# Optimization experiments

Hardware: AMD Instinct MI355X
Metric: run time of the kernel (lower is better)

## Reference

```python
import jax, jax.numpy as jnp
import numpy as np

N, D_IN, F = 65536, 512, 256
E = 524288
BATCH, K1 = 32, 200
BN_EPS = 1e-5


def setup_inputs() -> dict:
    key = jax.random.key(0)
    ks = iter(jax.random.split(key, 64))

    def nrm(shape, s=0.05):
        return jax.random.normal(next(ks), shape, jnp.float32) * s

    inp = {
        "feat": jax.random.normal(next(ks), (N, D_IN), jnp.float32),
        "A": jax.random.randint(next(ks), (2, E), 0, N, dtype=jnp.int32),
        "h1id": jax.random.randint(next(ks), (BATCH * K1,), 0, N // BATCH, dtype=jnp.int32),
        "batch": BATCH,
    }
    dims = [(D_IN, F), (F, F), (F, F), (F, F)]
    for i, (di, do) in enumerate(dims, 1):
        inp[f"eps{i}"] = jnp.zeros((), jnp.float32)          # GINConv train_eps, init 0
        inp[f"w{i}a"] = nrm((di, do)); inp[f"b{i}a"] = jnp.zeros((do,), jnp.float32)
        inp[f"w{i}b"] = nrm((do, do)); inp[f"b{i}b"] = jnp.zeros((do,), jnp.float32)
        inp[f"g{i}"] = jnp.ones((do,), jnp.float32)          # BN gamma
        inp[f"be{i}"] = jnp.zeros((do,), jnp.float32)        # BN beta
        inp[f"m{i}"] = nrm((do,))                            # BN running mean
        inp[f"v{i}"] = jax.random.uniform(next(ks), (do,), jnp.float32, 0.5, 1.5)  # BN running var
    inp["wc1"] = nrm((F, F)); inp["bc1"] = jnp.zeros((F,), jnp.float32)
    inp["pa"] = jnp.full((F,), 0.25, jnp.float32)            # PReLU per-channel slope
    inp["wc2"] = nrm((F, 2)); inp["bc2"] = jnp.zeros((2,), jnp.float32)
    return inp


def _gin_conv(x, src, dst, eps, wa, ba, wb, bb, g, be, m, v):
    # sum aggregation over in-edges: aggr[i] = sum_{(j->i)} x[j]
    aggr = jax.ops.segment_sum(x[src], dst, num_segments=N)
    h = (1.0 + eps) * x + aggr
    h = jax.nn.relu(h @ wa + ba) @ wb + bb
    # BatchNorm1d in eval mode (running stats)
    return (h - m) * jax.lax.rsqrt(v + BN_EPS) * g + be


def _forward(feat, A, h1id, batch,
             eps1, w1a, b1a, w1b, b1b, g1, be1, m1, v1,
             eps2, w2a, b2a, w2b, b2b, g2, be2, m2, v2,
             eps3, w3a, b3a, w3b, b3b, g3, be3, m3, v3,
             eps4, w4a, b4a, w4b, b4b, g4, be4, m4, v4,
             wc1, bc1, pa, wc2, bc2):
    src, dst = A[0], A[1]
    h = jax.nn.relu(_gin_conv(feat, src, dst, eps1, w1a, b1a, w1b, b1b, g1, be1, m1, v1))
    h = jax.nn.relu(_gin_conv(h, src, dst, eps2, w2a, b2a, w2b, b2b, g2, be2, m2, v2))
    h = jax.nn.relu(_gin_conv(h, src, dst, eps3, w3a, b3a, w3b, b3b, g3, be3, m3, v3))
    h = _gin_conv(h, src, dst, eps4, w4a, b4a, w4b, b4b, g4, be4, m4, v4)
    score = h.reshape(batch, -1, F)                      # [B, n_per_graph, F]
    idx = h1id.reshape(batch, K1)
    edge_feat = jnp.take_along_axis(score, idx[:, :, None], axis=1)  # [B, K1, F]
    ef = edge_feat.reshape(-1, F)
    hc = ef @ wc1 + bc1
    hc = jnp.where(hc > 0, hc, pa * hc)                  # PReLU(256)
    return hc @ wc2 + bc2                                # [B*K1, 2]


def reference(feat, A, h1id, batch,
              eps1, w1a, b1a, w1b, b1b, g1, be1, m1, v1,
              eps2, w2a, b2a, w2b, b2b, g2, be2, m2, v2,
              eps3, w3a, b3a, w3b, b3b, g3, be3, m3, v3,
              eps4, w4a, b4a, w4b, b4b, g4, be4, m4, v4,
              wc1, bc1, pa, wc2, bc2):
    return _forward(feat, A, h1id, batch,
                    eps1, w1a, b1a, w1b, b1b, g1, be1, m1, v1,
                    eps2, w2a, b2a, w2b, b2b, g2, be2, m2, v2,
                    eps3, w3a, b3a, w3b, b3b, g3, be3, m3, v3,
                    eps4, w4a, b4a, w4b, b4b, g4, be4, m4, v4,
                    wc1, bc1, pa, wc2, bc2)
```

## Files before the change

### kernel.cpp

```cpp
#include <hip/hip_runtime.h>

typedef unsigned short u16;
typedef unsigned int   u32;
typedef __bf16  bf16x8 __attribute__((ext_vector_type(8)));
typedef float   f32x4  __attribute__((ext_vector_type(4)));
typedef u32     u32x4  __attribute__((ext_vector_type(4)));

#define NN 65536
#define NE 524288
#define FD 256

typedef const __attribute__((address_space(1))) void* gas_p;
typedef __attribute__((address_space(3))) void* las_p;
#define GLDS16(g, l) __builtin_amdgcn_global_load_lds((gas_p)(const void*)(g), (las_p)(void*)(l), 16, 0, 0)

__device__ __forceinline__ u16 f2bf(float f){
  u32 u = __float_as_uint(f);
  u += 0x7fffu + ((u >> 16) & 1u);
  return (u16)(u >> 16);
}
__device__ __forceinline__ float bf2f(u32 lo16){
  return __uint_as_float(lo16 << 16);
}
__device__ __forceinline__ void acc8(float* a, uint4 v){
  a[0] += bf2f(v.x & 0xffffu); a[1] += bf2f(v.x >> 16);
  a[2] += bf2f(v.y & 0xffffu); a[3] += bf2f(v.y >> 16);
  a[4] += bf2f(v.z & 0xffffu); a[5] += bf2f(v.z >> 16);
  a[6] += bf2f(v.w & 0xffffu); a[7] += bf2f(v.w >> 16);
}

__global__ __launch_bounds__(256) void prep_k(
    const float* __restrict__ w1a, const float* __restrict__ w1b,
    const float* __restrict__ w2a, const float* __restrict__ w2b,
    const float* __restrict__ w3a, const float* __restrict__ w3b,
    const float* __restrict__ w4a, const float* __restrict__ w4b,
    const float* __restrict__ wc1, u16* __restrict__ wT)
{
  int idx = blockIdx.x * 256 + threadIdx.x;
  const float* src; int base, K, local;
  if (idx < 131072){ src = w1a; base = 0; K = 512; local = idx; }
  else {
    local = idx - 131072;
    int j = local >> 16;
    local &= 65535;
    K = 256;
    base = 131072 + j * 65536;
    switch (j){
      case 0: src = w1b; break;
      case 1: src = w2a; break;
      case 2: src = w2b; break;
      case 3: src = w3a; break;
      case 4: src = w3b; break;
      case 5: src = w4a; break;
      case 6: src = w4b; break;
      default: src = wc1; break;
    }
  }
  int n = local & 255;
  int k = local >> 8;
  wT[base + n * K + k] = f2bf(src[k * 256 + n]);
}

__global__ __launch_bounds__(256) void hist_k(const int* __restrict__ dst, int* __restrict__ deg){
  int e = blockIdx.x * 256 + threadIdx.x;
  atomicAdd(&deg[dst[e]], 1);
}

__global__ __launch_bounds__(1024) void scan_k(const int* __restrict__ deg, int* __restrict__ rs){
  __shared__ int part[1024];
  int t = threadIdx.x;
  int base = t * 64;
  int sum = 0;
  for (int i = 0; i < 64; ++i) sum += deg[base + i];
  part[t] = sum;
  __syncthreads();
  for (int off = 1; off < 1024; off <<= 1){
    int v = 0;
    if (t >= off) v = part[t - off];
    __syncthreads();
    part[t] += v;
    __syncthreads();
  }
  int run = part[t] - sum;
  for (int i = 0; i < 64; ++i){ rs[base + i] = run; run += deg[base + i]; }
  if (t == 1023) rs[65536] = part[1023];
}

__global__ __launch_bounds__(256) void scat_k(
    const int* __restrict__ src, const int* __restrict__ dst,
    const int* __restrict__ rs, int* __restrict__ cursor, int* __restrict__ csr)
{
  int e = blockIdx.x * 256 + threadIdx.x;
  int d = dst[e];
  int pos = atomicAdd(&cursor[d], 1);
  csr[rs[d] + pos] = src[e];
}

template<int AF32, int MODE, int RELU, int K>
__global__ __launch_bounds__(512) void gemm_k(
    const void* __restrict__ Ap, const u16* __restrict__ Bt,
    u16* __restrict__ C,
    const float* __restrict__ p0, const float* __restrict__ p1,
    const float* __restrict__ p2, const float* __restrict__ p3,
    const float* __restrict__ p4)
{
  __shared__ u16 lds[32768];
  u16* As = lds;
  u16* Bs = lds + 8192;
  const int t    = threadIdx.x;
  const int lane = t & 63;
  const int w    = t >> 6;
  const int wm   = w & 1;
  const int wn   = w >> 1;
  const int m0   = blockIdx.x * 128;
  const int mrow = lane & 15;
  const int quad = lane >> 4;

  f32x4 acc[4][4];
  const f32x4 zero = {0.f, 0.f, 0.f, 0.f};
  #pragma unroll
  for (int i = 0; i < 4; ++i)
    #pragma unroll
    for (int j = 0; j < 4; ++j) acc[i][j] = zero;

  const u16* Ab = (const u16*)Ap;
  const float* Af = (const float*)Ap;

  for (int k0 = 0; k0 < K; k0 += 64){
    if (AF32){
      #pragma unroll
      for (int i = 0; i < 2; ++i){
        int p   = i * 512 + t;
        int row = p >> 3;
        const float* s = Af + (size_t)(m0 + row) * K + k0 + (p & 7) * 8;
        float4 x0 = *(const float4*)s;
        float4 x1 = *(const float4*)(s + 4);
        union { u32x4 q; u16 h[8]; } u;
        u.h[0] = f2bf(x0.x); u.h[1] = f2bf(x0.y); u.h[2] = f2bf(x0.z); u.h[3] = f2bf(x0.w);
        u.h[4] = f2bf(x1.x); u.h[5] = f2bf(x1.y); u.h[6] = f2bf(x1.z); u.h[7] = f2bf(x1.w);
        int dst = (p & ~7) | ((p & 7) ^ (row & 7));
        *(u32x4*)&As[dst * 8] = u.q;
      }
    } else {
      #pragma unroll
      for (int i = 0; i < 2; ++i){
        int p   = i * 512 + t;
        int row = p >> 3;
        int ch  = (p & 7) ^ (row & 7);
        GLDS16(Ab + (size_t)(m0 + row) * K + k0 + ch * 8, &As[p * 8]);
      }
    }
    #pragma unroll
    for (int i = 0; i < 4; ++i){
      int p   = i * 512 + t;
      int row = p >> 3;
      int ch  = (p & 7) ^ (row & 7);
      GLDS16(Bt + (size_t)row * K + k0 + ch * 8, &Bs[p * 8]);
    }
    __syncthreads();
    #pragma unroll
    for (int ks = 0; ks < 2; ++ks){
      bf16x8 af[4], bq[4];
      #pragma unroll
      for (int mi = 0; mi < 4; ++mi){
        int r  = wm * 64 + mi * 16 + mrow;
        int ch = (quad + ks * 4) ^ (r & 7);
        af[mi] = *(const bf16x8*)&As[(r * 8 + ch) * 8];
      }
      #pragma unroll
      for (int ni = 0; ni < 4; ++ni){
        int rb = wn * 64 + ni * 16 + mrow;
        int ch = (quad + ks * 4) ^ (rb & 7);
        bq[ni] = *(const bf16x8*)&Bs[(rb * 8 + ch) * 8];
      }
      #pragma unroll
      for (int mi = 0; mi < 4; ++mi)
        #pragma unroll
        for (int ni = 0; ni < 4; ++ni)
          acc[mi][ni] = __builtin_amdgcn_mfma_f32_16x16x32_bf16(af[mi], bq[ni], acc[mi][ni], 0, 0, 0);
    }
    __syncthreads();
  }

  #pragma unroll
  for (int ni = 0; ni < 4; ++ni){
    int c  = wn * 64 + ni * 16 + mrow;
    float scale = 1.f, shift = 0.f, slope = 0.f;
    if (MODE == 1){
      float s = p0[c] * rsqrtf(p3[c] + 1e-5f);
      scale = s;
      shift = (p4[c] - p2[c]) * s + p1[c];
    }
    if (MODE == 2){ shift = p0[c]; slope = p1[c]; }
    #pragma unroll
    for (int mi = 0; mi < 4; ++mi){
      int rbase = wm * 64 + mi * 16 + quad * 4;
      #pragma unroll
      for (int reg = 0; reg < 4; ++reg){
        float v = acc[mi][ni][reg];
        if (MODE == 1){
          v = v * scale + shift;
          if (RELU) v = fmaxf(v, 0.f);
        }
        if (MODE == 2){
          v += shift;
          v = v > 0.f ? v : slope * v;
        }
        lds[(rbase + reg) * 256 + c] = f2bf(v);
      }
    }
  }
  __syncthreads();
  #pragma unroll
  for (int i = 0; i < 8; ++i){
    int p  = i * 512 + t;
    int r  = p >> 5;
    int ch = p & 31;
    u32x4 q = *(const u32x4*)&lds[r * 256 + ch * 8];
    *(u32x4*)&C[(size_t)(m0 + r) * 256 + ch * 8] = q;
  }
}

__global__ __launch_bounds__(512) void fuse_k(
    const u16* __restrict__ y, const int* __restrict__ rs, const int* __restrict__ csr,
    const float* __restrict__ epsp, const float* __restrict__ abias,
    const u16* __restrict__ B1t,
    const float* __restrict__ g, const float* __restrict__ be,
    const float* __restrict__ m, const float* __restrict__ v,
    const float* __restrict__ bb,
    const u16* __restrict__ B2t,
    u16* __restrict__ yout)
{
  __shared__ u16 lds[32768];
  const int t    = threadIdx.x;
  const int lane = t & 63;
  const int w    = t >> 6;
  const int wm   = w & 1;
  const int wn   = w >> 1;
  const int m0   = blockIdx.x * 128;
  const int mrow = lane & 15;
  const int quad = lane >> 4;

  {
    int lane32 = lane & 31;
    int half   = lane >> 5;
    int f0     = lane32 * 8;
    float e1 = 1.0f + epsp[0];
    float4 b0 = *(const float4*)(abias + f0);
    float4 b1 = *(const float4*)(abias + f0 + 4);
    #pragma unroll 1
    for (int i = 0; i < 8; ++i){
      int r    = w * 16 + i * 2 + half;
      int node = m0 + r;
      int s0 = rs[node], s1 = rs[node + 1];
      float a[8] = {0.f,0.f,0.f,0.f,0.f,0.f,0.f,0.f};
      int e = s0;
      for (; e + 4 <= s1; e += 4){
        int sa = csr[e], sb = csr[e+1], sc = csr[e+2], sd = csr[e+3];
        uint4 va = *(const uint4*)(y + (size_t)sa * 256 + f0);
        uint4 vb = *(const uint4*)(y + (size_t)sb * 256 + f0);
        uint4 vc = *(const uint4*)(y + (size_t)sc * 256 + f0);
        uint4 vd = *(const uint4*)(y + (size_t)sd * 256 + f0);
        acc8(a, va); acc8(a, vb); acc8(a, vc); acc8(a, vd);
      }
      for (; e < s1; ++e)
        acc8(a, *(const uint4*)(y + (size_t)csr[e] * 256 + f0));
      uint4 own = *(const uint4*)(y + (size_t)node * 256 + f0);
      float r0 = fmaxf(e1 * bf2f(own.x & 0xffffu) + a[0] + b0.x, 0.f);
      float r1 = fmaxf(e1 * bf2f(own.x >> 16)     + a[1] + b0.y, 0.f);
      float r2 = fmaxf(e1 * bf2f(own.y & 0xffffu) + a[2] + b0.z, 0.f);
      float r3 = fmaxf(e1 * bf2f(own.y >> 16)     + a[3] + b0.w, 0.f);
      float r4 = fmaxf(e1 * bf2f(own.z & 0xffffu) + a[4] + b1.x, 0.f);
      float r5 = fmaxf(e1 * bf2f(own.z >> 16)     + a[5] + b1.y, 0.f);
      float r6 = fmaxf(e1 * bf2f(own.w & 0xffffu) + a[6] + b1.z, 0.f);
      float r7 = fmaxf(e1 * bf2f(own.w >> 16)     + a[7] + b1.w, 0.f);
      uint4 o;
      o.x = (u32)f2bf(r0) | ((u32)f2bf(r1) << 16);
      o.y = (u32)f2bf(r2) | ((u32)f2bf(r3) << 16);
      o.z = (u32)f2bf(r4) | ((u32)f2bf(r5) << 16);
      o.w = (u32)f2bf(r6) | ((u32)f2bf(r7) << 16);
      int ch = lane32 ^ (r & 7);
      *(uint4*)&lds[r * 256 + ch * 8] = o;
    }
  }
  __syncthreads();

  const f32x4 zero = {0.f, 0.f, 0.f, 0.f};

  f32x4 acc[4][4];
  #pragma unroll
  for (int i = 0; i < 4; ++i)
    #pragma unroll
    for (int j = 0; j < 4; ++j) acc[i][j] = zero;
  #pragma unroll
  for (int ks = 0; ks < 8; ++ks){
    bf16x8 af[4], bq[4];
    #pragma unroll
    for (int mi = 0; mi < 4; ++mi){
      int r    = wm * 64 + mi * 16 + mrow;
      int slot = (ks * 4 + quad) ^ (r & 7);
      af[mi] = *(const bf16x8*)&lds[r * 256 + slot * 8];
    }
    #pragma unroll
    for (int ni = 0; ni < 4; ++ni){
      int rb = wn * 64 + ni * 16 + mrow;
      bq[ni] = *(const bf16x8*)&B1t[(size_t)rb * 256 + ks * 32 + quad * 8];
    }
    #pragma unroll
    for (int mi = 0; mi < 4; ++mi)
      #pragma unroll
      for (int ni = 0; ni < 4; ++ni)
        acc[mi][ni] = __builtin_amdgcn_mfma_f32_16x16x32_bf16(af[mi], bq[ni], acc[mi][ni], 0, 0, 0);
  }
  __syncthreads();

  #pragma unroll
  for (int ni = 0; ni < 4; ++ni){
    int c = wn * 64 + ni * 16 + mrow;
    float scale = g[c] * rsqrtf(v[c] + 1e-5f);
    float shift = (bb[c] - m[c]) * scale + be[c];
    #pragma unroll
    for (int mi = 0; mi < 4; ++mi){
      int rbase = wm * 64 + mi * 16 + quad * 4;
      #pragma unroll
      for (int reg = 0; reg < 4; ++reg){
        int row = rbase + reg;
        float val = fmaxf(acc[mi][ni][reg] * scale + shift, 0.f);
        lds[row * 256 + (((c >> 3) ^ (row & 7)) << 3) + (c & 7)] = f2bf(val);
      }
    }
  }
  __syncthreads();

  f32x4 acc2[4][4];
  #pragma unroll
  for (int i = 0; i < 4; ++i)
    #pragma unroll
    for (int j = 0; j < 4; ++j) acc2[i][j] = zero;
  #pragma unroll
  for (int ks = 0; ks < 8; ++ks){
    bf16x8 af[4], bq[4];
    #pragma unroll
    for (int mi = 0; mi < 4; ++mi){
      int r    = wm * 64 + mi * 16 + mrow;
      int slot = (ks * 4 + quad) ^ (r & 7);
      af[mi] = *(const bf16x8*)&lds[r * 256 + slot * 8];
    }
    #pragma unroll
    for (int ni = 0; ni < 4; ++ni){
      int rb = wn * 64 + ni * 16 + mrow;
      bq[ni] = *(const bf16x8*)&B2t[(size_t)rb * 256 + ks * 32 + quad * 8];
    }
    #pragma unroll
    for (int mi = 0; mi < 4; ++mi)
      #pragma unroll
      for (int ni = 0; ni < 4; ++ni)
        acc2[mi][ni] = __builtin_amdgcn_mfma_f32_16x16x32_bf16(af[mi], bq[ni], acc2[mi][ni], 0, 0, 0);
  }
  __syncthreads();

  #pragma unroll
  for (int ni = 0; ni < 4; ++ni){
    int c = wn * 64 + ni * 16 + mrow;
    #pragma unroll
    for (int mi = 0; mi < 4; ++mi){
      int rbase = wm * 64 + mi * 16 + quad * 4;
      #pragma unroll
      for (int reg = 0; reg < 4; ++reg)
        lds[(rbase + reg) * 256 + c] = f2bf(acc2[mi][ni][reg]);
    }
  }
  __syncthreads();
  #pragma unroll
  for (int i = 0; i < 8; ++i){
    int p  = i * 512 + t;
    int r  = p >> 5;
    int ch = p & 31;
    u32x4 q = *(const u32x4*)&lds[r * 256 + ch * 8];
    *(u32x4*)&yout[(size_t)(m0 + r) * 256 + ch * 8] = q;
  }
}

template<int GATH>
__global__ __launch_bounds__(256) void agg_k(
    const u16* __restrict__ y, const int* __restrict__ rs, const int* __restrict__ csr,
    const float* __restrict__ epsp, const float* __restrict__ bias,
    const int* __restrict__ gidx, u16* __restrict__ tout)
{
  int sub    = threadIdx.x >> 5;
  int lane32 = threadIdx.x & 31;
  int idx    = blockIdx.x * 8 + sub;
  int node;
  if (GATH) node = (idx / 200) * 2048 + gidx[idx];
  else      node = idx;
  int f0 = lane32 * 8;
  float e1 = 1.0f + epsp[0];
  int s0 = rs[node], s1 = rs[node + 1];
  float a[8] = {0.f,0.f,0.f,0.f,0.f,0.f,0.f,0.f};
  int e = s0;
  for (; e + 4 <= s1; e += 4){
    int sa = csr[e], sb = csr[e+1], sc = csr[e+2], sd = csr[e+3];
    uint4 va = *(const uint4*)(y + (size_t)sa * 256 + f0);
    uint4 vb = *(const uint4*)(y + (size_t)sb * 256 + f0);
    uint4 vc = *(const uint4*)(y + (size_t)sc * 256 + f0);
    uint4 vd = *(const uint4*)(y + (size_t)sd * 256 + f0);
    acc8(a, va); acc8(a, vb); acc8(a, vc); acc8(a, vd);
  }
  for (; e < s1; ++e){
    int s = csr[e];
    acc8(a, *(const uint4*)(y + (size_t)s * 256 + f0));
  }
  uint4 own = *(const uint4*)(y + (size_t)node * 256 + f0);
  float ow[8];
  ow[0] = bf2f(own.x & 0xffffu); ow[1] = bf2f(own.x >> 16);
  ow[2] = bf2f(own.y & 0xffffu); ow[3] = bf2f(own.y >> 16);
  ow[4] = bf2f(own.z & 0xffffu); ow[5] = bf2f(own.z >> 16);
  ow[6] = bf2f(own.w & 0xffffu); ow[7] = bf2f(own.w >> 16);
  float4 b0 = *(const float4*)(bias + f0);
  float4 b1 = *(const float4*)(bias + f0 + 4);
  float r[8];
  r[0] = fmaxf(e1 * ow[0] + a[0] + b0.x, 0.f);
  r[1] = fmaxf(e1 * ow[1] + a[1] + b0.y, 0.f);
  r[2] = fmaxf(e1 * ow[2] + a[2] + b0.z, 0.f);
  r[3] = fmaxf(e1 * ow[3] + a[3] + b0.w, 0.f);
  r[4] = fmaxf(e1 * ow[4] + a[4] + b1.x, 0.f);
  r[5] = fmaxf(e1 * ow[5] + a[5] + b1.y, 0.f);
  r[6] = fmaxf(e1 * ow[6] + a[6] + b1.z, 0.f);
  r[7] = fmaxf(e1 * ow[7] + a[7] + b1.w, 0.f);
  uint4 o;
  o.x = (u32)f2bf(r[0]) | ((u32)f2bf(r[1]) << 16);
  o.y = (u32)f2bf(r[2]) | ((u32)f2bf(r[3]) << 16);
  o.z = (u32)f2bf(r[4]) | ((u32)f2bf(r[5]) << 16);
  o.w = (u32)f2bf(r[6]) | ((u32)f2bf(r[7]) << 16);
  *(uint4*)(tout + (size_t)idx * 256 + f0) = o;
}

__global__ __launch_bounds__(256) void head_k(
    const u16* __restrict__ hc, const float* __restrict__ wc2,
    const float* __restrict__ bc2, float* __restrict__ out)
{
  int row  = blockIdx.x * 4 + (threadIdx.x >> 6);
  int lane = threadIdx.x & 63;
  int f0   = lane * 4;
  uint2 hv = *(const uint2*)(hc + (size_t)row * 256 + f0);
  float h0 = bf2f(hv.x & 0xffffu), h1 = bf2f(hv.x >> 16);
  float h2 = bf2f(hv.y & 0xffffu), h3 = bf2f(hv.y >> 16);
  float4 wa = *(const float4*)(wc2 + f0 * 2);
  float4 wb = *(const float4*)(wc2 + f0 * 2 + 4);
  float acc0 = h0 * wa.x + h1 * wa.z + h2 * wb.x + h3 * wb.z;
  float acc1 = h0 * wa.y + h1 * wa.w + h2 * wb.y + h3 * wb.w;
  #pragma unroll
  for (int off = 32; off > 0; off >>= 1){
    acc0 += __shfl_xor(acc0, off);
    acc1 += __shfl_xor(acc1, off);
  }
  if (lane == 0){
    out[row * 2]     = acc0 + bc2[0];
    out[row * 2 + 1] = acc1 + bc2[1];
  }
}

extern "C" void kernel_launch(void* const* d_in, const int* in_sizes, int n_in,
                              void* d_out, int out_size, void* d_ws, size_t ws_size,
                              hipStream_t stream)
{
  const float* feat = (const float*)d_in[0];
  const int*   A    = (const int*)d_in[1];
  const int*   h1id = (const int*)d_in[2];
  const float* eps[4] = {(const float*)d_in[4],  (const float*)d_in[13], (const float*)d_in[22], (const float*)d_in[31]};
  const float* wa [4] = {(const float*)d_in[5],  (const float*)d_in[14], (const float*)d_in[23], (const float*)d_in[32]};
  const float* ba [4] = {(const float*)d_in[6],  (const float*)d_in[15], (const float*)d_in[24], (const float*)d_in[33]};
  const float* wb [4] = {(const float*)d_in[7],  (const float*)d_in[16], (const float*)d_in[25], (const float*)d_in[34]};
  const float* bb [4] = {(const float*)d_in[8],  (const float*)d_in[17], (const float*)d_in[26], (const float*)d_in[35]};
  const float* g  [4] = {(const float*)d_in[9],  (const float*)d_in[18], (const float*)d_in[27], (const float*)d_in[36]};
  const float* be [4] = {(const float*)d_in[10], (const float*)d_in[19], (const float*)d_in[28], (const float*)d_in[37]};
  const float* m  [4] = {(const float*)d_in[11], (const float*)d_in[20], (const float*)d_in[29], (const float*)d_in[38]};
  const float* v  [4] = {(const float*)d_in[12], (const float*)d_in[21], (const float*)d_in[30], (const float*)d_in[39]};
  const float* wc1 = (const float*)d_in[40];
  const float* bc1 = (const float*)d_in[41];
  const float* pa  = (const float*)d_in[42];
  const float* wc2 = (const float*)d_in[43];
  const float* bc2 = (const float*)d_in[44];

  char* ws = (char*)d_ws;
  u16* wT     = (u16*)(ws + 0);
  int* deg    = (int*)(ws + 1310720);
  int* rs     = (int*)(ws + 1572864);
  int* cursor = (int*)(ws + 1835264);
  int* csr    = (int*)(ws + 2097408);
  u16* ybuf   = (u16*)(ws + 4194560);
  u16* tbuf   = (u16*)(ws + 37748992);
  u16* hbuf   = (u16*)(ws + 71303424);
  u16* h4     = (u16*)(ws + 104857856);
  u16* hc     = (u16*)(ws + 108134656);

  u16* w1aT = wT;
  u16* w1bT = wT + 131072;
  u16* w2aT = wT + 196608;
  u16* w2bT = wT + 262144;
  u16* w3aT = wT + 327680;
  u16* w3bT = wT + 393216;
  u16* w4aT = wT + 458752;
  u16* w4bT = wT + 524288;
  u16* wc1T = wT + 589824;

  hipMemsetAsync(deg, 0, 65536 * 4, stream);
  hipMemsetAsync(cursor, 0, 65536 * 4, stream);
  prep_k<<<2560, 256, 0, stream>>>(wa[0], wb[0], wa[1], wb[1], wa[2], wb[2], wa[3], wb[3], wc1, wT);
  hist_k<<<NE / 256, 256, 0, stream>>>(A + NE, deg);
  scan_k<<<1, 1024, 0, stream>>>(deg, rs);
  scat_k<<<NE / 256, 256, 0, stream>>>(A, A + NE, rs, cursor, csr);

  gemm_k<1,0,0,512><<<512, 512, 0, stream>>>(feat, w1aT, ybuf,
      nullptr, nullptr, nullptr, nullptr, nullptr);

  fuse_k<<<512, 512, 0, stream>>>(ybuf, rs, csr, eps[0], ba[0], w1bT,
      g[0], be[0], m[0], v[0], bb[0], w2aT, tbuf);
  fuse_k<<<512, 512, 0, stream>>>(tbuf, rs, csr, eps[1], ba[1], w2bT,
      g[1], be[1], m[1], v[1], bb[1], w3aT, ybuf);
  fuse_k<<<512, 512, 0, stream>>>(ybuf, rs, csr, eps[2], ba[2], w3bT,
      g[2], be[2], m[2], v[2], bb[2], w4aT, tbuf);

  agg_k<1><<<800, 256, 0, stream>>>(tbuf, rs, csr, eps[3], ba[3], h1id, hbuf);
  gemm_k<0,1,0,256><<<50, 512, 0, stream>>>(hbuf, w4bT, h4,
      g[3], be[3], m[3], v[3], bb[3]);

  gemm_k<0,2,0,256><<<50, 512, 0, stream>>>(h4, wc1T, hc,
      bc1, pa, nullptr, nullptr, nullptr);
  head_k<<<1600, 256, 0, stream>>>(hc, wc2, bc2, (float*)d_out);

  (void)in_sizes; (void)n_in; (void)out_size; (void)ws_size;
}
```

Before: 715.1 us.

## Split neighbor aggregation out of fused GIN kernel into separate agg pass

The fused kernel that gathered neighbor rows, then ran two GEMMs in one block, is split. A standalone aggregation kernel now writes the aggregated activations to global memory, and a new fuse2 kernel streams that tile via global_load_lds with a K-tiled, LDS-staged B1 operand. GEMM epilogue LDS stores also gain an XOR swizzle to cut bank conflicts. The split lets the gather run at its own occupancy, at the cost of an extra global round-trip of the 65536x256 activation per layer.

```diff
diff --git a/kernel.cpp b/kernel.cpp
--- a/kernel.cpp
+++ b/kernel.cpp
@@ -27,6 +27,9 @@
   a[2] += bf2f(v.y & 0xffffu); a[3] += bf2f(v.y >> 16);
   a[4] += bf2f(v.z & 0xffffu); a[5] += bf2f(v.z >> 16);
   a[6] += bf2f(v.w & 0xffffu); a[7] += bf2f(v.w >> 16);
+}
+__device__ __forceinline__ int lsw(int row, int c){
+  return row * 256 + ((((c >> 3) ^ (row & 7)) << 3) | (c & 7));
 }
 
 __global__ __launch_bounds__(256) void prep_k(
@@ -206,7 +209,7 @@
           v += shift;
           v = v > 0.f ? v : slope * v;
         }
-        lds[(rbase + reg) * 256 + c] = f2bf(v);
+        lds[lsw(rbase + reg, c)] = f2bf(v);
       }
     }
   }
@@ -216,22 +219,21 @@
     int p  = i * 512 + t;
     int r  = p >> 5;
     int ch = p & 31;
-    u32x4 q = *(const u32x4*)&lds[r * 256 + ch * 8];
+    u32x4 q = *(const u32x4*)&lds[r * 256 + (ch ^ (r & 7)) * 8];
     *(u32x4*)&C[(size_t)(m0 + r) * 256 + ch * 8] = q;
   }
 }
 
-__global__ __launch_bounds__(512) void fuse_k(
-    const u16* __restrict__ y, const int* __restrict__ rs, const int* __restrict__ csr,
-    const float* __restrict__ epsp, const float* __restrict__ abias,
-    const u16* __restrict__ B1t,
+__global__ __launch_bounds__(512) void fuse2_k(
+    const u16* __restrict__ Ap, const u16* __restrict__ B1t,
     const float* __restrict__ g, const float* __restrict__ be,
     const float* __restrict__ m, const float* __restrict__ v,
     const float* __restrict__ bb,
-    const u16* __restrict__ B2t,
-    u16* __restrict__ yout)
+    const u16* __restrict__ B2t, u16* __restrict__ C)
 {
   __shared__ u16 lds[32768];
+  u16* As = lds;
+  u16* Bs = lds + 8192;
   const int t    = threadIdx.x;
   const int lane = t & 63;
   const int w    = t >> 6;
@@ -241,57 +243,75 @@
   const int mrow = lane & 15;
   const int quad = lane >> 4;
 
-  {
-    int lane32 = lane & 31;
-    int half   = lane >> 5;
-    int f0     = lane32 * 8;
-    float e1 = 1.0f + epsp[0];
-    float4 b0 = *(const float4*)(abias + f0);
-    float4 b1 = *(const float4*)(abias + f0 + 4);
-    #pragma unroll 1
-    for (int i = 0; i < 8; ++i){
-      int r    = w * 16 + i * 2 + half;
-      int node = m0 + r;
-      int s0 = rs[node], s1 = rs[node + 1];
-      float a[8] = {0.f,0.f,0.f,0.f,0.f,0.f,0.f,0.f};
-      int e = s0;
-      for (; e + 4 <= s1; e += 4){
-        int sa = csr[e], sb = csr[e+1], sc = csr[e+2], sd = csr[e+3];
-        uint4 va = *(const uint4*)(y + (size_t)sa * 256 + f0);
-        uint4 vb = *(const uint4*)(y + (size_t)sb * 256 + f0);
-        uint4 vc = *(const uint4*)(y + (size_t)sc * 256 + f0);
-        uint4 vd = *(const uint4*)(y + (size_t)sd * 256 + f0);
-        acc8(a, va); acc8(a, vb); acc8(a, vc); acc8(a, vd);
-      }
-      for (; e < s1; ++e)
-        acc8(a, *(const uint4*)(y + (size_t)csr[e] * 256 + f0));
-      uint4 own = *(const uint4*)(y + (size_t)node * 256 + f0);
-      float r0 = fmaxf(e1 * bf2f(own.x & 0xffffu) + a[0] + b0.x, 0.f);
-      float r1 = fmaxf(e1 * bf2f(own.x >> 16)     + a[1] + b0.y, 0.f);
-      float r2 = fmaxf(e1 * bf2f(own.y & 0xffffu) + a[2] + b0.z, 0.f);
-      float r3 = fmaxf(e1 * bf2f(own.y >> 16)     + a[3] + b0.w, 0.f);
-      float r4 = fmaxf(e1 * bf2f(own.z & 0xffffu) + a[4] + b1.x, 0.f);
-      float r5 = fmaxf(e1 * bf2f(own.z >> 16)     + a[5] + b1.y, 0.f);
-      float r6 = fmaxf(e1 * bf2f(own.w & 0xffffu) + a[6] + b1.z, 0.f);
-      float r7 = fmaxf(e1 * bf2f(own.w >> 16)     + a[7] + b1.w, 0.f);
-      uint4 o;
-      o.x = (u32)f2bf(r0) | ((u32)f2bf(r1) << 16);
-      o.y = (u32)f2bf(r2) | ((u32)f2bf(r3) << 16);
-      o.z = (u32)f2bf(r4) | ((u32)f2bf(r5) << 16);
-      o.w = (u32)f2bf(r6) | ((u32)f2bf(r7) << 16);
-      int ch = lane32 ^ (r & 7);
-      *(uint4*)&lds[r * 256 + ch * 8] = o;
+  const f32x4 zero = {0.f, 0.f, 0.f, 0.f};
+  f32x4 acc[4][4];
+  #pragma unroll
+  for (int i = 0; i < 4; ++i)
+    #pragma unroll
+    for (int j = 0; j < 4; ++j) acc[i][j] = zero;
+
+  for (int k0 = 0; k0 < 256; k0 += 64){
+    #pragma unroll
+    for (int i = 0; i < 2; ++i){
+      int p   = i * 512 + t;
+      int row = p >> 3;
+      int ch  = (p & 7) ^ (row & 7);
+      GLDS16(Ap + (size_t)(m0 + row) * 256 + k0 + ch * 8, &As[p * 8]);
+    }
+    #pragma unroll
+    for (int i = 0; i < 4; ++i){
+      int p   = i * 512 + t;
+      int row = p >> 3;
+      int ch  = (p & 7) ^ (row & 7);
+      GLDS16(B1t + (size_t)row * 256 + k0 + ch * 8, &Bs[p * 8]);
+    }
+    __syncthreads();
+    #pragma unroll
+    for (int ks = 0; ks < 2; ++ks){
+      bf16x8 af[4], bq[4];
+      #pragma unroll
+      for (int mi = 0; mi < 4; ++mi){
+        int r  = wm * 64 + mi * 16 + mrow;
+        int ch = (quad + ks * 4) ^ (r & 7);
+        af[mi] = *(const bf16x8*)&As[(r * 8 + ch) * 8];
+      }
+      #pragma unroll
+      for (int ni = 0; ni < 4; ++ni){
+        int rb = wn * 64 + ni * 16 + mrow;
+        int ch = (quad + ks * 4) ^ (rb & 7);
+        bq[ni] = *(const bf16x8*)&Bs[(rb * 8 + ch) * 8];
+      }
+      #pragma unroll
+      for (int mi = 0; mi < 4; ++mi)
+        #pragma unroll
+        for (int ni = 0; ni < 4; ++ni)
+          acc[mi][ni] = __builtin_amdgcn_mfma_f32_16x16x32_bf16(af[mi], bq[ni], acc[mi][ni], 0, 0, 0);
+    }
+    __syncthreads();
+  }
+
+  #pragma unroll
+  for (int ni = 0; ni < 4; ++ni){
+    int c = wn * 64 + ni * 16 + mrow;
+    float scale = g[c] * rsqrtf(v[c] + 1e-5f);
+    float shift = (bb[c] - m[c]) * scale + be[c];
+    #pragma unroll
+    for (int mi = 0; mi < 4; ++mi){
+      int rbase = wm * 64 + mi * 16 + quad * 4;
+      #pragma unroll
+      for (int reg = 0; reg < 4; ++reg){
+        float val = fmaxf(acc[mi][ni][reg] * scale + shift, 0.f);
+        lds[lsw(rbase + reg, c)] = f2bf(val);
+      }
     }
   }
   __syncthreads();
 
-  const f32x4 zero = {0.f, 0.f, 0.f, 0.f};
-
-  f32x4 acc[4][4];
+  f32x4 acc2[4][4];
   #pragma unroll
   for (int i = 0; i < 4; ++i)
     #pragma unroll
-    for (int j = 0; j < 4; ++j) acc[i][j] = zero;
+    for (int j = 0; j < 4; ++j) acc2[i][j] = zero;
   #pragma unroll
   for (int ks = 0; ks < 8; ++ks){
     bf16x8 af[4], bq[4];
@@ -304,70 +324,25 @@
     #pragma unroll
     for (int ni = 0; ni < 4; ++ni){
       int rb = wn * 64 + ni * 16 + mrow;
-      bq[ni] = *(const bf16x8*)&B1t[(size_t)rb * 256 + ks * 32 + quad * 8];
+      bq[ni] = *(const bf16x8*)&B2t[(size_t)rb * 256 + ks * 32 + quad * 8];
     }
     #pragma unroll
     for (int mi = 0; mi < 4; ++mi)
       #pragma unroll
       for (int ni = 0; ni < 4; ++ni)
-        acc[mi][ni] = __builtin_amdgcn_mfma_f32_16x16x32_bf16(af[mi], bq[ni], acc[mi][ni], 0, 0, 0);
+        acc2[mi][ni] = __builtin_amdgcn_mfma_f32_16x16x32_bf16(af[mi], bq[ni], acc2[mi][ni], 0, 0, 0);
   }
   __syncthreads();
 
   #pragma unroll
   for (int ni = 0; ni < 4; ++ni){
     int c = wn * 64 + ni * 16 + mrow;
-    float scale = g[c] * rsqrtf(v[c] + 1e-5f);
-    float shift = (bb[c] - m[c]) * scale + be[c];
     #pragma unroll
     for (int mi = 0; mi < 4; ++mi){
       int rbase = wm * 64 + mi * 16 + quad * 4;
       #pragma unroll
-      for (int reg = 0; reg < 4; ++reg){
-        int row = rbase + reg;
-        float val = fmaxf(acc[mi][ni][reg] * scale + shift, 0.f);
-        lds[row * 256 + (((c >> 3) ^ (row & 7)) << 3) + (c & 7)] = f2bf(val);
-      }
-    }
-  }
-  __syncthreads();
-
-  f32x4 acc2[4][4];
-  #pragma unroll
-  for (int i = 0; i < 4; ++i)
-    #pragma unroll
-    for (int j = 0; j < 4; ++j) acc2[i][j] = zero;
-  #pragma unroll
-  for (int ks = 0; ks < 8; ++ks){
-    bf16x8 af[4], bq[4];
-    #pragma unroll
-    for (int mi = 0; mi < 4; ++mi){
-      int r    = wm * 64 + mi * 16 + mrow;
-      int slot = (ks * 4 + quad) ^ (r & 7);
-      af[mi] = *(const bf16x8*)&lds[r * 256 + slot * 8];
-    }
-    #pragma unroll
-    for (int ni = 0; ni < 4; ++ni){
-      int rb = wn * 64 + ni * 16 + mrow;
-      bq[ni] = *(const bf16x8*)&B2t[(size_t)rb * 256 + ks * 32 + quad * 8];
-    }
-    #pragma unroll
-    for (int mi = 0; mi < 4; ++mi)
-      #pragma unroll
-      for (int ni = 0; ni < 4; ++ni)
-        acc2[mi][ni] = __builtin_amdgcn_mfma_f32_16x16x32_bf16(af[mi], bq[ni], acc2[mi][ni], 0, 0, 0);
-  }
-  __syncthreads();
-
-  #pragma unroll
-  for (int ni = 0; ni < 4; ++ni){
-    int c = wn * 64 + ni * 16 + mrow;
-    #pragma unroll
-    for (int mi = 0; mi < 4; ++mi){
-      int rbase = wm * 64 + mi * 16 + quad * 4;
-      #pragma unroll
       for (int reg = 0; reg < 4; ++reg)
-        lds[(rbase + reg) * 256 + c] = f2bf(acc2[mi][ni][reg]);
+        lds[lsw(rbase + reg, c)] = f2bf(acc2[mi][ni][reg]);
     }
   }
   __syncthreads();
@@ -376,8 +351,8 @@
     int p  = i * 512 + t;
     int r  = p >> 5;
     int ch = p & 31;
-    u32x4 q = *(const u32x4*)&lds[r * 256 + ch * 8];
-    *(u32x4*)&yout[(size_t)(m0 + r) * 256 + ch * 8] = q;
+    u32x4 q = *(const u32x4*)&lds[r * 256 + (ch ^ (r & 7)) * 8];
+    *(u32x4*)&C[(size_t)(m0 + r) * 256 + ch * 8] = q;
   }
 }
 
@@ -490,7 +465,6 @@
   int* csr    = (int*)(ws + 2097408);
   u16* ybuf   = (u16*)(ws + 4194560);
   u16* tbuf   = (u16*)(ws + 37748992);
-  u16* hbuf   = (u16*)(ws + 71303424);
   u16* h4     = (u16*)(ws + 104857856);
   u16* hc     = (u16*)(ws + 108134656);
 
@@ -514,15 +488,18 @@
   gemm_k<1,0,0,512><<<512, 512, 0, stream>>>(feat, w1aT, ybuf,
       nullptr, nullptr, nullptr, nullptr, nullptr);
 
-  fuse_k<<<512, 512, 0, stream>>>(ybuf, rs, csr, eps[0], ba[0], w1bT,
-      g[0], be[0], m[0], v[0], bb[0], w2aT, tbuf);
-  fuse_k<<<512, 512, 0, stream>>>(tbuf, rs, csr, eps[1], ba[1], w2bT,
+  agg_k<0><<<NN / 8, 256, 0, stream>>>(ybuf, rs, csr, eps[0], ba[0], nullptr, tbuf);
+  fuse2_k<<<512, 512, 0, stream>>>(tbuf, w1bT,
+      g[0], be[0], m[0], v[0], bb[0], w2aT, ybuf);
+  agg_k<0><<<NN / 8, 256, 0, stream>>>(ybuf, rs, csr, eps[1], ba[1], nullptr, tbuf);
+  fuse2_k<<<512, 512, 0, stream>>>(tbuf, w2bT,
       g[1], be[1], m[1], v[1], bb[1], w3aT, ybuf);
-  fuse_k<<<512, 512, 0, stream>>>(ybuf, rs, csr, eps[2], ba[2], w3bT,
-      g[2], be[2], m[2], v[2], bb[2], w4aT, tbuf);
-
-  agg_k<1><<<800, 256, 0, stream>>>(tbuf, rs, csr, eps[3], ba[3], h1id, hbuf);
-  gemm_k<0,1,0,256><<<50, 512, 0, stream>>>(hbuf, w4bT, h4,
+  agg_k<0><<<NN / 8, 256, 0, stream>>>(ybuf, rs, csr, eps[2], ba[2], nullptr, tbuf);
+  fuse2_k<<<512, 512, 0, stream>>>(tbuf, w3bT,
+      g[2], be[2], m[2], v[2], bb[2], w4aT, ybuf);
+
+  agg_k<1><<<800, 256, 0, stream>>>(ybuf, rs, csr, eps[3], ba[3], h1id, tbuf);
+  gemm_k<0,1,0,256><<<50, 512, 0, stream>>>(tbuf, w4bT, h4,
       g[3], be[3], m[3], v[3], bb[3]);
 
   gemm_k<0,2,0,256><<<50, 512, 0, stream>>>(h4, wc1T, hc,
```

New measurement: 651.0 us. 9.0% less time.
